# Performance work log

Measured on AMD Instinct MI355X. Metric: run time of the kernel, lower is better.

## Reference

```python
import jax, jax.numpy as jnp
import numpy as np

D_MODEL, N_HEADS, N_KV_HEADS = 2048, 16, 4
D_HEAD = D_MODEL // N_HEADS  # 128
N_REP = N_HEADS // N_KV_HEADS  # 4
B, S = 2, 2048
ROPE_THETA = 10000.0


def setup_inputs() -> dict:
    key = jax.random.key(0)
    ks = jax.random.split(key, 6)
    x = jax.random.normal(ks[0], (B, S, D_MODEL), dtype=jnp.float32)
    # RoPE frequencies (real/imag parts of freqs_cis)
    inv_freq = 1.0 / (ROPE_THETA ** (np.arange(0, D_HEAD, 2, dtype=np.float32) / D_HEAD))
    angles = np.arange(S, dtype=np.float32)[:, None] * inv_freq[None, :]  # [S, D_HEAD//2]
    freqs_cos = jnp.asarray(np.cos(angles))
    freqs_sin = jnp.asarray(np.sin(angles))
    # causal additive mask [1,1,S,S]
    causal = jnp.tril(jnp.ones((S, S), dtype=bool))
    mask = jnp.where(causal, 0.0, -1e9).astype(jnp.float32)[None, None]
    scale = 0.02
    wq = jax.random.normal(ks[1], (D_MODEL, N_HEADS * D_HEAD), dtype=jnp.float32) * scale
    wk = jax.random.normal(ks[2], (D_MODEL, N_KV_HEADS * D_HEAD), dtype=jnp.float32) * scale
    wv = jax.random.normal(ks[3], (D_MODEL, N_KV_HEADS * D_HEAD), dtype=jnp.float32) * scale
    wo = jax.random.normal(ks[4], (N_HEADS * D_HEAD, D_MODEL), dtype=jnp.float32) * scale
    return {"x": x, "freqs_cos": freqs_cos, "freqs_sin": freqs_sin, "mask": mask,
            "wq": wq, "wk": wk, "wv": wv, "wo": wo}


def _apply_rope(t, cos, sin):
    # t: [B, S, H, D]; cos/sin: [S, D//2] -> complex rotation on interleaved pairs
    tr = t.reshape(*t.shape[:-1], -1, 2)
    xr, xi = tr[..., 0], tr[..., 1]
    c = cos[None, :, None, :]
    s = sin[None, :, None, :]
    out_r = xr * c - xi * s
    out_i = xr * s + xi * c
    return jnp.stack([out_r, out_i], axis=-1).reshape(t.shape)


def reference(x, freqs_cos, freqs_sin, mask, wq, wk, wv, wo):
    b, s, _ = x.shape
    xq = (x @ wq).reshape(b, s, N_HEADS, D_HEAD)
    xk = (x @ wk).reshape(b, s, N_KV_HEADS, D_HEAD)
    xv = (x @ wv).reshape(b, s, N_KV_HEADS, D_HEAD)
    xq = _apply_rope(xq, freqs_cos, freqs_sin)
    xk = _apply_rope(xk, freqs_cos, freqs_sin)
    # GQA: repeat each kv head n_rep times (head h uses kv head h // n_rep)
    xk = jnp.repeat(xk, N_REP, axis=2)  # [B,S,H,D]
    xv = jnp.repeat(xv, N_REP, axis=2)
    scores = jnp.einsum("bshd,bthd->bhst", xq, xk) / jnp.sqrt(jnp.float32(D_HEAD))
    scores = scores + mask
    probs = jax.nn.softmax(scores, axis=-1)
    out = jnp.einsum("bhst,bthd->bshd", probs, xv).reshape(b, s, N_HEADS * D_HEAD)
    return out @ wo
```

## Files before the change

kernel.cpp:

```cpp
#include <hip/hip_runtime.h>
#include <hip/hip_bf16.h>

#define BB 2
#define SS 2048
#define DM 2048
#define NH 16
#define NKV 4
#define DH 128
#define QS 3072

typedef __hip_bfloat16 bf16;
typedef short short8 __attribute__((ext_vector_type(8)));
typedef float floatx4 __attribute__((ext_vector_type(4)));

__device__ __forceinline__ bf16 f2b(float v) { return __float2bfloat16(v); }
__device__ __forceinline__ short f2bs(float v) {
    bf16 t = __float2bfloat16(v);
    return __builtin_bit_cast(short, t);
}
__device__ __forceinline__ void store_c(bf16* p, float v) { *p = __float2bfloat16(v); }
__device__ __forceinline__ void store_c(float* p, float v) { *p = v; }

__global__ __launch_bounds__(256) void convert_x(const float4* __restrict__ x,
                                                 bf16* __restrict__ xb, int n4) {
    int i = blockIdx.x * blockDim.x + threadIdx.x;
    if (i >= n4) return;
    float4 v = x[i];
    bf16* p = xb + (size_t)i * 4;
    p[0] = f2b(v.x); p[1] = f2b(v.y); p[2] = f2b(v.z); p[3] = f2b(v.w);
}

__global__ __launch_bounds__(256) void convert_wT(const float* __restrict__ w,
                                                  bf16* __restrict__ outT,
                                                  int N, int Kd) {
    const int n0 = blockIdx.x * 64, k0 = blockIdx.y * 64;
    __shared__ float tile[64][65];
    const int tid = threadIdx.x;
    for (int i = tid; i < 4096; i += 256) {
        int r = i >> 6, c = i & 63;
        tile[r][c] = w[(size_t)(k0 + r) * N + n0 + c];
    }
    __syncthreads();
    for (int i = tid; i < 4096; i += 256) {
        int r = i >> 6, c = i & 63;
        outT[(size_t)(n0 + r) * Kd + k0 + c] = f2b(tile[c][r]);
    }
}

template <typename TC>
__global__ __launch_bounds__(256) void mfma_gemm(const bf16* __restrict__ A,
                                                 const bf16* __restrict__ BT,
                                                 TC* __restrict__ C,
                                                 int M, int N, int K) {
    __shared__ short As[128 * 32];
    __shared__ short Bs[128 * 32];
    const int tid = threadIdx.x;
    const int w = tid >> 6, lane = tid & 63;
    const int col16 = lane & 15, quad = lane >> 4;
    const int row0 = blockIdx.y * 128, col0 = blockIdx.x * 128;
    const int wr0 = (w >> 1) * 64, wc0 = (w & 1) * 64;

    floatx4 acc[4][4];
    #pragma unroll
    for (int mi = 0; mi < 4; mi++)
        #pragma unroll
        for (int ni = 0; ni < 4; ni++) acc[mi][ni] = (floatx4){0.f, 0.f, 0.f, 0.f};

    for (int k0 = 0; k0 < K; k0 += 32) {
        __syncthreads();
        #pragma unroll
        for (int it = 0; it < 2; it++) {
            int c = w * 128 + it * 64 + lane;
            int r = c >> 2, seg = c & 3;
            const bf16* g = A + (size_t)(row0 + r) * K + k0 + seg * 8;
            __builtin_amdgcn_global_load_lds(
                (const __attribute__((address_space(1))) unsigned int*)g,
                (__attribute__((address_space(3))) unsigned int*)&As[(w * 128 + it * 64) * 8],
                16, 0, 0);
        }
        #pragma unroll
        for (int it = 0; it < 2; it++) {
            int c = w * 128 + it * 64 + lane;
            int r = c >> 2, seg = c & 3;
            const bf16* g = BT + (size_t)(col0 + r) * K + k0 + seg * 8;
            __builtin_amdgcn_global_load_lds(
                (const __attribute__((address_space(1))) unsigned int*)g,
                (__attribute__((address_space(3))) unsigned int*)&Bs[(w * 128 + it * 64) * 8],
                16, 0, 0);
        }
        __syncthreads();

        short8 af[4], bfr[4];
        #pragma unroll
        for (int mi = 0; mi < 4; mi++)
            af[mi] = *(const short8*)&As[(wr0 + mi * 16 + col16) * 32 + quad * 8];
        #pragma unroll
        for (int ni = 0; ni < 4; ni++)
            bfr[ni] = *(const short8*)&Bs[(wc0 + ni * 16 + col16) * 32 + quad * 8];
        #pragma unroll
        for (int mi = 0; mi < 4; mi++)
            #pragma unroll
            for (int ni = 0; ni < 4; ni++)
                acc[mi][ni] = __builtin_amdgcn_mfma_f32_16x16x32_bf16(af[mi], bfr[ni], acc[mi][ni], 0, 0, 0);
    }
    #pragma unroll
    for (int mi = 0; mi < 4; mi++)
        #pragma unroll
        for (int ni = 0; ni < 4; ni++)
            #pragma unroll
            for (int r = 0; r < 4; r++)
                store_c(&C[(size_t)(row0 + wr0 + mi * 16 + quad * 4 + r) * N +
                           col0 + wc0 + ni * 16 + col16],
                        acc[mi][ni][r]);
}

__global__ void rope_kernel(bf16* __restrict__ base, const float* __restrict__ cs,
                            const float* __restrict__ sn, int n_heads, int total) {
    int idx = blockIdx.x * blockDim.x + threadIdx.x;
    if (idx >= total) return;
    int i = idx & 63;
    int h = (idx >> 6) % n_heads;
    size_t bs = (size_t)idx / (64 * n_heads);
    int s = (int)(bs % SS);
    float c = cs[s * 64 + i];
    float si = sn[s * 64 + i];
    bf16* p = base + bs * QS + h * DH + 2 * i;
    float xr = __bfloat162float(p[0]), xi = __bfloat162float(p[1]);
    p[0] = f2b(xr * c - xi * si);
    p[1] = f2b(xr * si + xi * c);
}

__global__ __launch_bounds__(256) void transpose_v(const bf16* __restrict__ qkv,
                                                   bf16* __restrict__ vt) {
    const int s0 = blockIdx.x * 64, d0 = blockIdx.y * 64;
    const int b = blockIdx.z >> 2, kvh = blockIdx.z & 3;
    __shared__ bf16 tile[64][65];
    const int tid = threadIdx.x;
    for (int i = tid; i < 4096; i += 256) {
        int r = i >> 6, c = i & 63;
        tile[r][c] = qkv[(size_t)(b * SS + s0 + r) * QS + 2560 + kvh * DH + d0 + c];
    }
    __syncthreads();
    for (int i = tid; i < 4096; i += 256) {
        int r = i >> 6, c = i & 63;
        vt[((size_t)(b * NKV + kvh) * DH + d0 + r) * SS + s0 + c] = tile[c][r];
    }
}

#define PPAD 72

__global__ __launch_bounds__(256) void flash_attn(const bf16* __restrict__ qkv,
                                                  const bf16* __restrict__ vt,
                                                  bf16* __restrict__ ao) {
    const int bx = blockIdx.x, h = blockIdx.y, b = blockIdx.z;
    const int kvh = h >> 2;
    __shared__ short Ks[2][64 * 128];
    __shared__ short Vs[2][128 * 64];
    __shared__ short Ps[4 * 16 * PPAD];
    const int tid = threadIdx.x;
    const int w = tid >> 6, lane = tid & 63;
    const int col = lane & 15, quad = lane >> 4;
    const int c7 = col & 7;
    const float scale = 0.08838834764831845f;

    const int krl = lane >> 4, kseg = lane & 15;
    const int vrl = lane >> 3, vseg = lane & 7;

    const bf16* kgb = qkv + (size_t)b * SS * QS + 2048 + kvh * DH;
    const bf16* vgb = vt + (size_t)(b * NKV + kvh) * DH * SS;

    for (int phase = 0; phase < 2; phase++) {
        const int qt = phase == 0 ? bx : (SS / 64 - 1 - bx);
        const int q0 = qt * 64;

        short8 aq[4];
        const bf16* qbase = qkv + (size_t)(b * SS + q0 + w * 16 + col) * QS + h * DH;
        #pragma unroll
        for (int kc = 0; kc < 4; kc++)
            aq[kc] = *(const short8*)(qbase + kc * 32 + quad * 8);

        floatx4 o[8];
        #pragma unroll
        for (int dt = 0; dt < 8; dt++) o[dt] = (floatx4){0.f, 0.f, 0.f, 0.f};
        float mrow[4] = {-3e38f, -3e38f, -3e38f, -3e38f};
        float lrow[4] = {0.f, 0.f, 0.f, 0.f};

        for (int kt = 0; kt <= qt; kt++) {
            const int cur = kt & 1;
            __syncthreads();
            if (kt == 0) {
                #pragma unroll
                for (int it = 0; it < 4; it++) {
                    int row = w * 16 + it * 4 + krl;
                    const bf16* g = kgb + (size_t)row * QS + ((kseg ^ (row & 7)) * 8);
                    __builtin_amdgcn_global_load_lds(
                        (const __attribute__((address_space(1))) unsigned int*)g,
                        (__attribute__((address_space(3))) unsigned int*)&Ks[0][(w * 16 + it * 4) * 128],
                        16, 0, 0);
                }
                #pragma unroll
                for (int it = 0; it < 4; it++) {
                    int drow = w * 32 + it * 8 + vrl;
                    const bf16* g = vgb + (size_t)drow * SS + ((vseg ^ (drow & 7)) * 8);
                    __builtin_amdgcn_global_load_lds(
                        (const __attribute__((address_space(1))) unsigned int*)g,
                        (__attribute__((address_space(3))) unsigned int*)&Vs[0][(w * 32 + it * 8) * 64],
                        16, 0, 0);
                }
                __syncthreads();
            }
            if (kt < qt) {
                const int nk0 = (kt + 1) * 64;
                #pragma unroll
                for (int it = 0; it < 4; it++) {
                    int row = w * 16 + it * 4 + krl;
                    const bf16* g = kgb + (size_t)(nk0 + row) * QS + ((kseg ^ (row & 7)) * 8);
                    __builtin_amdgcn_global_load_lds(
                        (const __attribute__((address_space(1))) unsigned int*)g,
                        (__attribute__((address_space(3))) unsigned int*)&Ks[cur ^ 1][(w * 16 + it * 4) * 128],
                        16, 0, 0);
                }
                #pragma unroll
                for (int it = 0; it < 4; it++) {
                    int drow = w * 32 + it * 8 + vrl;
                    const bf16* g = vgb + (size_t)drow * SS + nk0 + ((vseg ^ (drow & 7)) * 8);
                    __builtin_amdgcn_global_load_lds(
                        (const __attribute__((address_space(1))) unsigned int*)g,
                        (__attribute__((address_space(3))) unsigned int*)&Vs[cur ^ 1][(w * 32 + it * 8) * 64],
                        16, 0, 0);
                }
            }

            const int k0 = kt * 64;
            floatx4 s[4];
            __builtin_amdgcn_s_setprio(1);
            #pragma unroll
            for (int n = 0; n < 4; n++) {
                s[n] = (floatx4){0.f, 0.f, 0.f, 0.f};
                #pragma unroll
                for (int kc = 0; kc < 4; kc++) {
                    short8 bk = *(const short8*)&Ks[cur][(n * 16 + col) * 128 + (((kc * 4 + quad) ^ c7) * 8)];
                    s[n] = __builtin_amdgcn_mfma_f32_16x16x32_bf16(aq[kc], bk, s[n], 0, 0, 0);
                }
            }
            __builtin_amdgcn_s_setprio(0);

            #pragma unroll
            for (int n = 0; n < 4; n++)
                #pragma unroll
                for (int r = 0; r < 4; r++) {
                    float v = s[n][r] * scale;
                    if (kt == qt && (k0 + n * 16 + col) > (q0 + w * 16 + quad * 4 + r)) v = -3e38f;
                    s[n][r] = v;
                }
            float alpha[4];
            #pragma unroll
            for (int r = 0; r < 4; r++) {
                float rm = fmaxf(fmaxf(s[0][r], s[1][r]), fmaxf(s[2][r], s[3][r]));
                rm = fmaxf(rm, __shfl_xor(rm, 1));
                rm = fmaxf(rm, __shfl_xor(rm, 2));
                rm = fmaxf(rm, __shfl_xor(rm, 4));
                rm = fmaxf(rm, __shfl_xor(rm, 8));
                float mn = fmaxf(mrow[r], rm);
                alpha[r] = __expf(mrow[r] - mn);
                mrow[r] = mn;
                float rs = 0.f;
                #pragma unroll
                for (int n = 0; n < 4; n++) {
                    float p = __expf(s[n][r] - mn);
                    s[n][r] = p;
                    rs += p;
                }
                rs += __shfl_xor(rs, 1);
                rs += __shfl_xor(rs, 2);
                rs += __shfl_xor(rs, 4);
                rs += __shfl_xor(rs, 8);
                lrow[r] = lrow[r] * alpha[r] + rs;
            }
            short* pw = &Ps[w * 16 * PPAD];
            #pragma unroll
            for (int n = 0; n < 4; n++)
                #pragma unroll
                for (int r = 0; r < 4; r++)
                    pw[(quad * 4 + r) * PPAD + n * 16 + col] = f2bs(s[n][r]);
            #pragma unroll
            for (int dt = 0; dt < 8; dt++)
                #pragma unroll
                for (int r = 0; r < 4; r++) o[dt][r] *= alpha[r];
            short8 ap0 = *(const short8*)&pw[col * PPAD + quad * 8];
            short8 ap1 = *(const short8*)&pw[col * PPAD + 32 + quad * 8];
            __builtin_amdgcn_s_setprio(1);
            #pragma unroll
            for (int dt = 0; dt < 8; dt++) {
                short8 bv0 = *(const short8*)&Vs[cur][(dt * 16 + col) * 64 + ((quad ^ c7) * 8)];
                o[dt] = __builtin_amdgcn_mfma_f32_16x16x32_bf16(ap0, bv0, o[dt], 0, 0, 0);
                short8 bv1 = *(const short8*)&Vs[cur][(dt * 16 + col) * 64 + (((quad + 4) ^ c7) * 8)];
                o[dt] = __builtin_amdgcn_mfma_f32_16x16x32_bf16(ap1, bv1, o[dt], 0, 0, 0);
            }
            __builtin_amdgcn_s_setprio(0);
        }
        #pragma unroll
        for (int r = 0; r < 4; r++) {
            float inv = 1.f / lrow[r];
            int srow = q0 + w * 16 + quad * 4 + r;
            bf16* op = ao + ((size_t)(b * SS + srow) * NH + h) * DH;
            #pragma unroll
            for (int dt = 0; dt < 8; dt++)
                op[dt * 16 + col] = f2b(o[dt][r] * inv);
        }
    }
}

extern "C" void kernel_launch(void* const* d_in, const int* in_sizes, int n_in,
                              void* d_out, int out_size, void* d_ws, size_t ws_size,
                              hipStream_t stream) {
    const float* x  = (const float*)d_in[0];
    const float* fc = (const float*)d_in[1];
    const float* fs = (const float*)d_in[2];
    const float* wq = (const float*)d_in[4];
    const float* wk = (const float*)d_in[5];
    const float* wv = (const float*)d_in[6];
    const float* wo = (const float*)d_in[7];
    float* out = (float*)d_out;

    const int M = BB * SS;
    bf16* qkv    = (bf16*)d_ws;
    bf16* xb     = qkv + (size_t)M * QS;
    bf16* wqkvT  = xb + (size_t)M * DM;
    bf16* ao     = xb;
    bf16* vt     = wqkvT;
    bf16* woT    = qkv;

    dim3 blk(256);
    convert_x<<<(M * DM / 4 + 255) / 256, blk, 0, stream>>>((const float4*)x, xb, M * DM / 4);
    convert_wT<<<dim3(DM / 64, DM / 64), blk, 0, stream>>>(wq, wqkvT, DM, DM);
    convert_wT<<<dim3((NKV * DH) / 64, DM / 64), blk, 0, stream>>>(wk, wqkvT + (size_t)2048 * DM, NKV * DH, DM);
    convert_wT<<<dim3((NKV * DH) / 64, DM / 64), blk, 0, stream>>>(wv, wqkvT + (size_t)2560 * DM, NKV * DH, DM);

    mfma_gemm<bf16><<<dim3(QS / 128, M / 128), blk, 0, stream>>>(xb, wqkvT, qkv, M, QS, DM);

    const int totq = BB * SS * NH * 64;
    const int totk = BB * SS * NKV * 64;
    rope_kernel<<<(totq + 255) / 256, blk, 0, stream>>>(qkv, fc, fs, NH, totq);
    rope_kernel<<<(totk + 255) / 256, blk, 0, stream>>>(qkv + 2048, fc, fs, NKV, totk);

    transpose_v<<<dim3(SS / 64, DH / 64, BB * NKV), blk, 0, stream>>>(qkv, vt);

    flash_attn<<<dim3(SS / 128, NH, BB), blk, 0, stream>>>(qkv, vt, ao);

    convert_wT<<<dim3(DM / 64, DM / 64), blk, 0, stream>>>(wo, woT, DM, DM);
    mfma_gemm<float><<<dim3(DM / 128, M / 128), blk, 0, stream>>>(ao, woT, out, M, DM, DM);
}
```

Before: 379.2 us.

## Streamline flash softmax: exp2 with folded scale, MFMA row sums, conditional rescale

Folds the 1/sqrt(d) scale and log2(e) into one constant and uses the hardware exp2 with an FMA, removing a multiply pass over the scores. The row-sum shuffle reduction is replaced by two extra MFMAs of P against a ones vector, so the denominator uses the same bf16-rounded probabilities as the numerator. Rescaling of the output accumulators is skipped when no row max in the wavefront grew. This trims VALU and cross-lane work in the softmax. In exchange it adds two MFMAs per tile and a wave-uniform branch.

```diff
diff --git a/kernel.cpp b/kernel.cpp
--- a/kernel.cpp
+++ b/kernel.cpp
@@ -12,6 +12,12 @@
 typedef __hip_bfloat16 bf16;
 typedef short short8 __attribute__((ext_vector_type(8)));
 typedef float floatx4 __attribute__((ext_vector_type(4)));
+
+#if __has_builtin(__builtin_amdgcn_exp2f)
+#define EX2(x) __builtin_amdgcn_exp2f(x)
+#else
+#define EX2(x) exp2f(x)
+#endif
 
 __device__ __forceinline__ bf16 f2b(float v) { return __float2bfloat16(v); }
 __device__ __forceinline__ short f2bs(float v) {
@@ -161,13 +167,15 @@
     const int w = tid >> 6, lane = tid & 63;
     const int col = lane & 15, quad = lane >> 4;
     const int c7 = col & 7;
-    const float scale = 0.08838834764831845f;
+    const float C = 0.12751746517859245f;
 
     const int krl = lane >> 4, kseg = lane & 15;
     const int vrl = lane >> 3, vseg = lane & 7;
 
     const bf16* kgb = qkv + (size_t)b * SS * QS + 2048 + kvh * DH;
     const bf16* vgb = vt + (size_t)(b * NKV + kvh) * DH * SS;
+
+    const short8 vone = {0x3F80, 0x3F80, 0x3F80, 0x3F80, 0x3F80, 0x3F80, 0x3F80, 0x3F80};
 
     for (int phase = 0; phase < 2; phase++) {
         const int qt = phase == 0 ? bx : (SS / 64 - 1 - bx);
@@ -182,8 +190,8 @@
         floatx4 o[8];
         #pragma unroll
         for (int dt = 0; dt < 8; dt++) o[dt] = (floatx4){0.f, 0.f, 0.f, 0.f};
+        floatx4 oL = (floatx4){0.f, 0.f, 0.f, 0.f};
         float mrow[4] = {-3e38f, -3e38f, -3e38f, -3e38f};
-        float lrow[4] = {0.f, 0.f, 0.f, 0.f};
 
         for (int kt = 0; kt <= qt; kt++) {
             const int cur = kt & 1;
@@ -245,15 +253,15 @@
             }
             __builtin_amdgcn_s_setprio(0);
 
-            #pragma unroll
-            for (int n = 0; n < 4; n++)
-                #pragma unroll
-                for (int r = 0; r < 4; r++) {
-                    float v = s[n][r] * scale;
-                    if (kt == qt && (k0 + n * 16 + col) > (q0 + w * 16 + quad * 4 + r)) v = -3e38f;
-                    s[n][r] = v;
-                }
-            float alpha[4];
+            if (kt == qt) {
+                #pragma unroll
+                for (int n = 0; n < 4; n++)
+                    #pragma unroll
+                    for (int r = 0; r < 4; r++)
+                        if ((k0 + n * 16 + col) > (q0 + w * 16 + quad * 4 + r)) s[n][r] = -3e38f;
+            }
+
+            float rmx[4];
             #pragma unroll
             for (int r = 0; r < 4; r++) {
                 float rm = fmaxf(fmaxf(s[0][r], s[1][r]), fmaxf(s[2][r], s[3][r]));
@@ -261,32 +269,36 @@
                 rm = fmaxf(rm, __shfl_xor(rm, 2));
                 rm = fmaxf(rm, __shfl_xor(rm, 4));
                 rm = fmaxf(rm, __shfl_xor(rm, 8));
-                float mn = fmaxf(mrow[r], rm);
-                alpha[r] = __expf(mrow[r] - mn);
-                mrow[r] = mn;
-                float rs = 0.f;
-                #pragma unroll
-                for (int n = 0; n < 4; n++) {
-                    float p = __expf(s[n][r] - mn);
-                    s[n][r] = p;
-                    rs += p;
-                }
-                rs += __shfl_xor(rs, 1);
-                rs += __shfl_xor(rs, 2);
-                rs += __shfl_xor(rs, 4);
-                rs += __shfl_xor(rs, 8);
-                lrow[r] = lrow[r] * alpha[r] + rs;
-            }
+                rmx[r] = fmaxf(rm, mrow[r]);
+            }
+            bool grow = (rmx[0] > mrow[0]) | (rmx[1] > mrow[1]) |
+                        (rmx[2] > mrow[2]) | (rmx[3] > mrow[3]);
+            if (__any((int)grow)) {
+                float al[4];
+                #pragma unroll
+                for (int r = 0; r < 4; r++) {
+                    al[r] = EX2((mrow[r] - rmx[r]) * C);
+                    mrow[r] = rmx[r];
+                }
+                #pragma unroll
+                for (int dt = 0; dt < 8; dt++)
+                    #pragma unroll
+                    for (int r = 0; r < 4; r++) o[dt][r] *= al[r];
+                #pragma unroll
+                for (int r = 0; r < 4; r++) oL[r] *= al[r];
+            }
+            float mC[4];
+            #pragma unroll
+            for (int r = 0; r < 4; r++) mC[r] = mrow[r] * C;
+
             short* pw = &Ps[w * 16 * PPAD];
             #pragma unroll
             for (int n = 0; n < 4; n++)
                 #pragma unroll
                 for (int r = 0; r < 4; r++)
-                    pw[(quad * 4 + r) * PPAD + n * 16 + col] = f2bs(s[n][r]);
-            #pragma unroll
-            for (int dt = 0; dt < 8; dt++)
-                #pragma unroll
-                for (int r = 0; r < 4; r++) o[dt][r] *= alpha[r];
+                    pw[(quad * 4 + r) * PPAD + n * 16 + col] =
+                        f2bs(EX2(__builtin_fmaf(s[n][r], C, -mC[r])));
+
             short8 ap0 = *(const short8*)&pw[col * PPAD + quad * 8];
             short8 ap1 = *(const short8*)&pw[col * PPAD + 32 + quad * 8];
             __builtin_amdgcn_s_setprio(1);
@@ -297,11 +309,13 @@
                 short8 bv1 = *(const short8*)&Vs[cur][(dt * 16 + col) * 64 + (((quad + 4) ^ c7) * 8)];
                 o[dt] = __builtin_amdgcn_mfma_f32_16x16x32_bf16(ap1, bv1, o[dt], 0, 0, 0);
             }
+            oL = __builtin_amdgcn_mfma_f32_16x16x32_bf16(ap0, vone, oL, 0, 0, 0);
+            oL = __builtin_amdgcn_mfma_f32_16x16x32_bf16(ap1, vone, oL, 0, 0, 0);
             __builtin_amdgcn_s_setprio(0);
         }
         #pragma unroll
         for (int r = 0; r < 4; r++) {
-            float inv = 1.f / lrow[r];
+            float inv = 1.f / oL[r];
             int srow = q0 + w * 16 + quad * 4 + r;
             bf16* op = ao + ((size_t)(b * SS + srow) * NH + h) * DH;
             #pragma unroll
```

Result: faster. 366.3 us (-3.4%).
